# Performance work log

Hardware: AMD Instinct MI355X
Metric: run time of the kernel (lower is better)

Reference implementation:

```python
import jax, jax.numpy as jnp
import numpy as np

B, L, D = 2, 4096, 128      # batch, seq_len, d_model
ED = 2 * D                  # d_inner (expand=2) = 256
N = 16                      # d_state
K = 4                       # d_conv
R = (D + 15) // 16          # dt_rank = 8
H = 2 * D                   # mlp hidden = 256


def setup_inputs() -> dict:
    key = jax.random.key(0)
    ks = jax.random.split(key, 20)
    s = 0.05
    inp = {
        "x": jax.random.normal(ks[0], (B, L, D), dtype=jnp.float32),
        # outer block LayerNorm (norm1)
        "norm1_g": jnp.ones((D,), jnp.float32),
        "norm1_b": jnp.zeros((D,), jnp.float32),
        # MambaLayer inner LayerNorm
        "inner_g": jnp.ones((D,), jnp.float32),
        "inner_b": jnp.zeros((D,), jnp.float32),
        # Mamba params
        "in_w": jax.random.normal(ks[1], (2 * ED, D), jnp.float32) * s,      # in_proj (no bias)
        "conv_w": jax.random.normal(ks[2], (ED, 1, K), jnp.float32) * s,     # depthwise conv
        "conv_b": jax.random.normal(ks[3], (ED,), jnp.float32) * s,
        "xproj_w": jax.random.normal(ks[4], (R + 2 * N, ED), jnp.float32) * s,  # x_proj (no bias)
        "dt_w": jax.random.normal(ks[5], (ED, R), jnp.float32) * s,
        "dt_b": jax.random.normal(ks[6], (ED,), jnp.float32) * s,
        "A_log": jnp.tile(jnp.log(jnp.arange(1, N + 1, dtype=jnp.float32)), (ED, 1)),  # [ED,N]
        "Dp": jnp.ones((ED,), jnp.float32),
        "out_w": jax.random.normal(ks[7], (D, ED), jnp.float32) * s,         # out_proj (no bias)
        # MLP
        "fc1_w": jax.random.normal(ks[8], (H, D), jnp.float32) * s,
        "fc1_b": jnp.zeros((H,), jnp.float32),
        "fc2_w": jax.random.normal(ks[9], (D, H), jnp.float32) * s,
        "fc2_b": jnp.zeros((D,), jnp.float32),
    }
    return inp


def _ln(x, g, b, eps=1e-5):
    m = jnp.mean(x, axis=-1, keepdims=True)
    v = jnp.mean((x - m) ** 2, axis=-1, keepdims=True)
    return (x - m) * jax.lax.rsqrt(v + eps) * g + b


def _mamba(x, in_w, conv_w, conv_b, xproj_w, dt_w, dt_b, A_log, Dp, out_w):
    # x: [B, L, D]
    xz = jnp.einsum('bld,ed->ble', x, in_w)          # [B,L,2*ED]
    u, z = jnp.split(xz, 2, axis=-1)                 # each [B,L,ED]
    # causal depthwise conv1d over L
    u_c = jnp.transpose(u, (0, 2, 1))                # [B,ED,L]
    u_c = jax.lax.conv_general_dilated(
        u_c, conv_w, window_strides=(1,), padding=[(K - 1, 0)],
        dimension_numbers=('NCH', 'OIH', 'NCH'), feature_group_count=ED)
    u = jax.nn.silu(jnp.transpose(u_c, (0, 2, 1)) + conv_b)   # [B,L,ED]
    # input-dependent dt, B, C
    dbc = jnp.einsum('ble,re->blr', u, xproj_w)      # [B,L,R+2N]
    dt, Bm, Cm = jnp.split(dbc, [R, R + N], axis=-1)
    delta = jax.nn.softplus(jnp.einsum('blr,er->ble', dt, dt_w) + dt_b)  # [B,L,ED]
    A = -jnp.exp(A_log)                              # [ED,N]
    deltaA = jnp.exp(jnp.einsum('ble,en->blen', delta, A))               # [B,L,ED,N]
    deltaBu = jnp.einsum('ble,bln,ble->blen', delta, Bm, u)              # [B,L,ED,N]
    # selective scan over L
    def step(h, inp):
        dA, dBu, Ct = inp                            # [B,ED,N],[B,ED,N],[B,N]
        h = dA * h + dBu
        y = jnp.einsum('ben,bn->be', h, Ct)
        return h, y
    h0 = jnp.zeros((B, ED, N), u.dtype)
    xs = (jnp.transpose(deltaA, (1, 0, 2, 3)),
          jnp.transpose(deltaBu, (1, 0, 2, 3)),
          jnp.transpose(Cm, (1, 0, 2)))
    _, ys = jax.lax.scan(step, h0, xs)               # [L,B,ED]
    y = jnp.transpose(ys, (1, 0, 2)) + u * Dp        # [B,L,ED]
    y = y * jax.nn.silu(z)
    return jnp.einsum('ble,de->bld', y, out_w)       # [B,L,D]


def reference(x, norm1_g, norm1_b, inner_g, inner_b, in_w, conv_w, conv_b,
              xproj_w, dt_w, dt_b, A_log, Dp, out_w, fc1_w, fc1_b, fc2_w, fc2_b):
    # attn branch: mamba(inner_LN(norm1(x)))
    a = _mamba(_ln(_ln(x, norm1_g, norm1_b), inner_g, inner_b),
               in_w, conv_w, conv_b, xproj_w, dt_w, dt_b, A_log, Dp, out_w)
    x = x + a
    # mlp branch (note: original applies norm1 again to updated x)
    h = _ln(x, norm1_g, norm1_b)
    h = jax.nn.gelu(jnp.einsum('bld,hd->blh', h, fc1_w) + fc1_b, approximate=False)
    h = jnp.einsum('blh,dh->bld', h, fc2_w) + fc2_b
    return x + h
```

## Files before the change

kernel.cpp:

```cpp
#include <hip/hip_runtime.h>
#include <hip/hip_bf16.h>
#include <math.h>

#define BB 2
#define LL 4096
#define DD 128
#define ED 256
#define NN 16
#define KK 4
#define RR 8
#define HH 256
#define NT (BB*LL)
#define NC 128
#define LC 32
#define NCS 256
#define LCS 16

#define LOG2E 1.4426950408889634f

typedef __attribute__((ext_vector_type(8))) short short8;
typedef __attribute__((ext_vector_type(8))) unsigned short ushort8v;
typedef __attribute__((ext_vector_type(4))) float floatx4;

__device__ __forceinline__ unsigned short f2bf(float f) {
  unsigned int b = __builtin_bit_cast(unsigned int, f);
  b += 0x7FFFu + ((b >> 16) & 1u);
  return (unsigned short)(b >> 16);
}

__device__ __forceinline__ float exp2_fast(float x) {
#if __has_builtin(__builtin_amdgcn_exp2f)
  return __builtin_amdgcn_exp2f(x);
#else
  return exp2f(x);
#endif
}

__device__ __forceinline__ ushort8v pack8(const float4& v0, const float4& v1) {
  ushort8v p;
  p[0]=f2bf(v0.x); p[1]=f2bf(v0.y); p[2]=f2bf(v0.z); p[3]=f2bf(v0.w);
  p[4]=f2bf(v1.x); p[5]=f2bf(v1.y); p[6]=f2bf(v1.z); p[7]=f2bf(v1.w);
  return p;
}

#define S_IN  65536
#define S_XP  10240
#define S_OUT 32768
#define S_F1  32768
#define S_F2  32768
__global__ __launch_bounds__(256) void prep_k(
    const float* __restrict__ in_w, const float* __restrict__ xpw,
    const float* __restrict__ out_w, const float* __restrict__ fc1_w,
    const float* __restrict__ fc2_w, unsigned short* __restrict__ wb) {
  const int o = (blockIdx.x*256 + threadIdx.x) * 8;
  const float* src;
  int off;
  if (o < S_IN)                          { src = in_w;  off = o; }
  else if (o < S_IN+S_XP)                { src = xpw;   off = o - S_IN; }
  else if (o < S_IN+S_XP+S_OUT)          { src = out_w; off = o - S_IN - S_XP; }
  else if (o < S_IN+S_XP+S_OUT+S_F1)     { src = fc1_w; off = o - S_IN - S_XP - S_OUT; }
  else                                   { src = fc2_w; off = o - S_IN - S_XP - S_OUT - S_F1; }
  const float4 v0 = *(const float4*)(src + off);
  const float4 v1 = *(const float4*)(src + off + 4);
  *(ushort8v*)(wb + o) = pack8(v0, v1);
}

__global__ __launch_bounds__(512, 4) void scan1m_k(
    const float* __restrict__ x,
    const float* __restrict__ g1, const float* __restrict__ b1,
    const float* __restrict__ g2, const float* __restrict__ b2,
    const unsigned short* __restrict__ wb_in,
    const float* __restrict__ cw, const float* __restrict__ cb,
    const unsigned short* __restrict__ wb_xp,
    const float* __restrict__ dtw, const float* __restrict__ dtb,
    const float* __restrict__ A_log,
    float* __restrict__ uc, float* __restrict__ dbc,
    float* __restrict__ delta, float* __restrict__ gate,
    float* __restrict__ cA, float* __restrict__ cH) {
  __shared__ __align__(16) unsigned char SM[44624];
  auto Atile = reinterpret_cast<unsigned short(*)[136]>(SM);
  auto As    = reinterpret_cast<unsigned short(*)[264]>(SM);
  auto ubuf  = reinterpret_cast<float(*)[257]>(SM + 8704);
  auto sdbc  = reinterpret_cast<float(*)[40]>(SM + 8704);
  auto sus   = reinterpret_cast<float(*)[256]>(SM + 28240);

  const int c2 = blockIdx.x, b = blockIdx.y;
  const int tid = threadIdx.x;
  const int t0 = b*LL + c2*LCS;
  const int wave = tid >> 6, lane = tid & 63;
  const int quad = lane >> 4, l16 = lane & 15;

  {
    const int lr = tid >> 2, lk = (tid & 3) * 32;
    if (lr < 32) {
      if (lr < 19 && !(c2 == 0 && lr < 3)) {
        const float* Ap = x + (size_t)(t0 - 3 + lr)*DD + lk;
        float4 av[8];
        float s = 0.f, sq = 0.f;
        #pragma unroll
        for (int g = 0; g < 8; g++) {
          av[g] = *(const float4*)(Ap + g*4);
          s  += av[g].x + av[g].y + av[g].z + av[g].w;
          sq += av[g].x*av[g].x + av[g].y*av[g].y + av[g].z*av[g].z + av[g].w*av[g].w;
        }
        s += __shfl_xor(s, 1);  s += __shfl_xor(s, 2);
        sq += __shfl_xor(sq, 1); sq += __shfl_xor(sq, 2);
        const float m1 = s * (1.f/128.f);
        const float rs1 = rsqrtf(sq*(1.f/128.f) - m1*m1 + 1e-5f);
        float s2 = 0.f, sq2 = 0.f;
        #pragma unroll
        for (int g = 0; g < 8; g++) {
          const float4 gg = *(const float4*)(g1 + lk + g*4);
          const float4 bb = *(const float4*)(b1 + lk + g*4);
          av[g].x = (av[g].x - m1)*rs1*gg.x + bb.x;
          av[g].y = (av[g].y - m1)*rs1*gg.y + bb.y;
          av[g].z = (av[g].z - m1)*rs1*gg.z + bb.z;
          av[g].w = (av[g].w - m1)*rs1*gg.w + bb.w;
          s2  += av[g].x + av[g].y + av[g].z + av[g].w;
          sq2 += av[g].x*av[g].x + av[g].y*av[g].y + av[g].z*av[g].z + av[g].w*av[g].w;
        }
        s2 += __shfl_xor(s2, 1);  s2 += __shfl_xor(s2, 2);
        sq2 += __shfl_xor(sq2, 1); sq2 += __shfl_xor(sq2, 2);
        const float m2 = s2 * (1.f/128.f);
        const float rs2 = rsqrtf(sq2*(1.f/128.f) - m2*m2 + 1e-5f);
        #pragma unroll
        for (int g = 0; g < 4; g++) {
          const float4 ga = *(const float4*)(g2 + lk + g*8);
          const float4 gb = *(const float4*)(g2 + lk + g*8 + 4);
          const float4 ba = *(const float4*)(b2 + lk + g*8);
          const float4 bbv= *(const float4*)(b2 + lk + g*8 + 4);
          ushort8v pa;
          pa[0] = f2bf((av[2*g].x   - m2)*rs2*ga.x + ba.x);
          pa[1] = f2bf((av[2*g].y   - m2)*rs2*ga.y + ba.y);
          pa[2] = f2bf((av[2*g].z   - m2)*rs2*ga.z + ba.z);
          pa[3] = f2bf((av[2*g].w   - m2)*rs2*ga.w + ba.w);
          pa[4] = f2bf((av[2*g+1].x - m2)*rs2*gb.x + bbv.x);
          pa[5] = f2bf((av[2*g+1].y - m2)*rs2*gb.y + bbv.y);
          pa[6] = f2bf((av[2*g+1].z - m2)*rs2*gb.z + bbv.z);
          pa[7] = f2bf((av[2*g+1].w - m2)*rs2*gb.w + bbv.w);
          *(ushort8v*)&Atile[lr][lk + g*8] = pa;
        }
      } else {
        const ushort8v zz = {};
        #pragma unroll
        for (int g = 0; g < 4; g++) *(ushort8v*)&Atile[lr][lk + g*8] = zz;
      }
    }
  }
  __syncthreads();

  {
    const int mt = wave >> 2;
    short8 af[4];
    #pragma unroll
    for (int ks = 0; ks < 4; ks++)
      af[ks] = *(const short8*)&Atile[mt*16 + l16][ks*32 + quad*8];
    #pragma unroll
    for (int j = 0; j < 8; j++) {
      const int ncol = ((wave & 3)*8 + j) * 16;
      floatx4 acc = {};
      #pragma unroll
      for (int ks = 0; ks < 4; ks++) {
        short8 bv = *(const short8*)(wb_in + (size_t)(ncol + l16)*DD + ks*32 + quad*8);
        acc = __builtin_amdgcn_mfma_f32_16x16x32_bf16(af[ks], bv, acc, 0, 0, 0);
      }
      const int coll = ncol + l16;
      if (ncol < 256) {
        #pragma unroll
        for (int rr = 0; rr < 4; rr++) {
          const int m = mt*16 + quad*4 + rr;
          if (m < 19) ubuf[m][coll] = acc[rr];
        }
      } else {
        #pragma unroll
        for (int rr = 0; rr < 4; rr++) {
          const int m = mt*16 + quad*4 + rr;
          if (m >= 3 && m < 19) {
            const float v = acc[rr];
            gate[(size_t)(t0 + m - 3)*ED + coll - 256] = v / (1.f + __expf(-v));
          }
        }
      }
    }
  }
  __syncthreads();

  {
    const int ch = tid & 255, tg = tid >> 8;
    const int i0 = tg * 8;
    const float4 w = *(const float4*)(cw + ch*4);
    const float cbe = cb[ch];
    float v0 = ubuf[i0][ch], v1 = ubuf[i0+1][ch], v2 = ubuf[i0+2][ch];
    #pragma unroll
    for (int k = 0; k < 8; k++) {
      const float cur = ubuf[i0+3+k][ch];
      const float a = cbe + v0*w.x + v1*w.y + v2*w.z + cur*w.w;
      const float s = a / (1.f + __expf(-a));
      const int i = i0 + k;
      As[i][ch] = f2bf(s);
      sus[i][ch] = s;
      uc[(size_t)(t0+i)*ED + ch] = s;
      v0 = v1; v1 = v2; v2 = cur;
    }
  }
  __syncthreads();

  if (wave < 3) {
    const int jn = (wave == 2) ? 24 : wave*16;
    floatx4 acc = {};
    #pragma unroll
    for (int ks = 0; ks < 8; ks++) {
      const int ko = ks*32 + quad*8;
      short8 a  = *(const short8*)&As[l16][ko];
      short8 bv = *(const short8*)(wb_xp + (size_t)(jn + l16)*ED + ko);
      acc = __builtin_amdgcn_mfma_f32_16x16x32_bf16(a, bv, acc, 0, 0, 0);
    }
    const int n = jn + l16;
    if (wave < 2 || l16 >= 8) {
      #pragma unroll
      for (int rr = 0; rr < 4; rr++) {
        const int m = quad*4 + rr;
        sdbc[m][n] = acc[rr];
        dbc[(size_t)(t0 + m)*40 + n] = acc[rr];
      }
    }
  }
  __syncthreads();

  {
    const int e = tid >> 1, half = tid & 1;
    const int n0 = half * 8;
    const float4 dw0 = *(const float4*)(dtw + e*RR);
    const float4 dw1 = *(const float4*)(dtw + e*RR + 4);
    const float db = dtb[e];
    const float4 a0 = *(const float4*)(A_log + e*NN + n0);
    const float4 a1 = *(const float4*)(A_log + e*NN + n0 + 4);
    float Aen[8] = {-__expf(a0.x)*LOG2E, -__expf(a0.y)*LOG2E,
                    -__expf(a0.z)*LOG2E, -__expf(a0.w)*LOG2E,
                    -__expf(a1.x)*LOG2E, -__expf(a1.y)*LOG2E,
                    -__expf(a1.z)*LOG2E, -__expf(a1.w)*LOG2E};
    float h[8] = {};
    float sumd = 0.f;
    for (int t = 0; t < LCS; t++) {
      const float4 q0 = *(const float4*)&sdbc[t][0];
      const float4 q1 = *(const float4*)&sdbc[t][4];
      const float aa = db
          + q0.x*dw0.x + q0.y*dw0.y + q0.z*dw0.z + q0.w*dw0.w
          + q1.x*dw1.x + q1.y*dw1.y + q1.z*dw1.z + q1.w*dw1.w;
      const float dv = (aa > 20.f) ? aa : log1pf(__expf(aa));
      if (half == 0) delta[(size_t)(t0+t)*ED + e] = dv;
      const float du = dv * sus[t][e];
      const float4 B0 = *(const float4*)&sdbc[t][RR + n0];
      const float4 B1 = *(const float4*)&sdbc[t][RR + n0 + 4];
      const float Bv[8] = {B0.x,B0.y,B0.z,B0.w,B1.x,B1.y,B1.z,B1.w};
      sumd += dv;
      #pragma unroll
      for (int j = 0; j < 8; j++)
        h[j] = exp2_fast(dv * Aen[j])*h[j] + Bv[j]*du;
    }
    const size_t base = (((size_t)c2*BB + b)*ED + e)*NN + n0;
    *(float4*)(cA + base)     = make_float4(exp2_fast(sumd*Aen[0]), exp2_fast(sumd*Aen[1]),
                                            exp2_fast(sumd*Aen[2]), exp2_fast(sumd*Aen[3]));
    *(float4*)(cA + base + 4) = make_float4(exp2_fast(sumd*Aen[4]), exp2_fast(sumd*Aen[5]),
                                            exp2_fast(sumd*Aen[6]), exp2_fast(sumd*Aen[7]));
    *(float4*)(cH + base)     = make_float4(h[0], h[1], h[2], h[3]);
    *(float4*)(cH + base + 4) = make_float4(h[4], h[5], h[6], h[7]);
  }
}

__global__ __launch_bounds__(256) void scan2p8_k(float* __restrict__ cA,
    const float* __restrict__ cH) {
  const int gt = blockIdx.x*256 + threadIdx.x;
  const int scan = gt >> 3;
  const int seg  = gt & 7;
  const int lane = threadIdx.x & 63;
  const int lb   = lane & ~7;
  const int b = scan >> 12;
  const size_t base = (size_t)b*ED*NN + (scan & 4095);
  const int c0 = seg * 32;

  float ap = 1.f, hs = 0.f;
  for (int g = 0; g < 2; g++) {
    float av[16], hv[16];
    #pragma unroll
    for (int i = 0; i < 16; i++) {
      const size_t idx = (size_t)(c0 + g*16 + i)*(BB*ED*NN) + base;
      av[i] = cA[idx]; hv[i] = cH[idx];
    }
    #pragma unroll
    for (int i = 0; i < 16; i++) {
      hs = av[i]*hs + hv[i];
      ap *= av[i];
    }
  }
  float h = 0.f;
  #pragma unroll
  for (int k = 0; k < 7; k++) {
    const float ak = __shfl(ap, lb + k);
    const float hk = __shfl(hs, lb + k);
    if (seg > k) h = ak*h + hk;
  }
  for (int g = 0; g < 2; g++) {
    float av[16], hv[16];
    #pragma unroll
    for (int i = 0; i < 16; i++) {
      const size_t idx = (size_t)(c0 + g*16 + i)*(BB*ED*NN) + base;
      av[i] = cA[idx]; hv[i] = cH[idx];
    }
    #pragma unroll
    for (int i = 0; i < 16; i++) {
      const size_t idx = (size_t)(c0 + g*16 + i)*(BB*ED*NN) + base;
      cA[idx] = h;
      h = av[i]*h + hv[i];
    }
  }
}

__global__ __launch_bounds__(1024) void tail9_k(
    const float* __restrict__ gate, const float* __restrict__ delta,
    const float* __restrict__ uc, const float* __restrict__ dbc,
    const float* __restrict__ cP, const float* __restrict__ A_log,
    const float* __restrict__ Dpv, const float* __restrict__ x,
    const float* __restrict__ g1, const float* __restrict__ b1,
    const unsigned short* __restrict__ wb_out,
    const unsigned short* __restrict__ wb_f1,
    const unsigned short* __restrict__ wb_f2,
    const float* __restrict__ fc1_b, const float* __restrict__ fc2_b,
    float* __restrict__ out) {
  __shared__ __align__(16) unsigned short Au[32][264];
  __shared__ float xs[32][132];
  __shared__ float sbc[32][32];

  const int c = blockIdx.x, b = blockIdx.y;
  const int t0 = b*LL + c*LC;
  const int tid = threadIdx.x;
  const int wave = tid >> 6, lane = tid & 63;
  const int quad = lane >> 4, l16 = lane & 15;

  if (tid < 256) {
    const int row = tid >> 3, c4 = (tid & 7) * 4;
    *(float4*)&sbc[row][c4] = *(const float4*)(dbc + (size_t)(t0 + row)*40 + RR + c4);
  }
  __syncthreads();

  {
    const int e = tid >> 2, q = tid & 3;
    const int n0 = q * 4;
    float Aen[4], h[4];
    {
      const float4 a0 = *(const float4*)(A_log + e*NN + n0);
      Aen[0]=-__expf(a0.x)*LOG2E; Aen[1]=-__expf(a0.y)*LOG2E;
      Aen[2]=-__expf(a0.z)*LOG2E; Aen[3]=-__expf(a0.w)*LOG2E;
      const float4 h0 = *(const float4*)(cP + (((size_t)(2*c)*BB + b)*ED + e)*NN + n0);
      h[0]=h0.x; h[1]=h0.y; h[2]=h0.z; h[3]=h0.w;
    }
    const float Dpe = Dpv[e];
    float pd[8], pu[8], pg[8];
    #pragma unroll
    for (int i = 0; i < 8; i++) {
      pd[i] = delta[(size_t)(t0+i)*ED + e];
      pu[i] = uc[(size_t)(t0+i)*ED + e];
      pg[i] = gate[(size_t)(t0+i)*ED + e];
    }
    for (int g4 = 0; g4 < 4; g4++) {
      float cd[8], cu[8], cg[8];
      #pragma unroll
      for (int i = 0; i < 8; i++) { cd[i]=pd[i]; cu[i]=pu[i]; cg[i]=pg[i]; }
      if (g4 < 3) {
        const int tn = t0 + (g4+1)*8;
        #pragma unroll
        for (int i = 0; i < 8; i++) {
          pd[i] = delta[(size_t)(tn+i)*ED + e];
          pu[i] = uc[(size_t)(tn+i)*ED + e];
          pg[i] = gate[(size_t)(tn+i)*ED + e];
        }
      }
      #pragma unroll
      for (int i = 0; i < 8; i++) {
        const int t = g4*8 + i;
        const float dv = cd[i];
        const float uv = cu[i];
        const float du = dv * uv;
        const float4 B0 = *(const float4*)&sbc[t][n0];
        const float4 C0 = *(const float4*)&sbc[t][16 + n0];
        const float Bv[4] = {B0.x,B0.y,B0.z,B0.w};
        const float Cv[4] = {C0.x,C0.y,C0.z,C0.w};
        float part = 0.f;
        #pragma unroll
        for (int j = 0; j < 4; j++) {
          h[j] = exp2_fast(dv * Aen[j])*h[j] + Bv[j]*du;
          part += h[j]*Cv[j];
        }
        part += __shfl_xor(part, 1);
        part += __shfl_xor(part, 2);
        if (q == 0)
          Au[t][e] = f2bf((part + uv*Dpe) * cg[i]);
      }
    }
  }
  __syncthreads();

  {
    const int mi = (wave & 1) * 16;
    const int wn = (wave >> 1) * 16;
    floatx4 acc = {};
    #pragma unroll
    for (int ks = 0; ks < 8; ks++) {
      const int ko = ks*32 + quad*8;
      short8 a  = *(const short8*)&Au[mi + l16][ko];
      short8 bv = *(const short8*)(wb_out + (size_t)(wn + l16)*ED + ko);
      acc = __builtin_amdgcn_mfma_f32_16x16x32_bf16(a, bv, acc, 0, 0, 0);
    }
    const int n = wn + l16;
    #pragma unroll
    for (int r = 0; r < 4; r++) {
      const int m = mi + quad*4 + r;
      xs[m][n] = acc[r] + x[(size_t)(t0 + m)*DD + n];
    }
  }
  __syncthreads();

  if (tid < 512) {
    const int lr = tid >> 4, le = (tid & 15) * 8;
    float vv[8];
    float s = 0.f, sq = 0.f;
    #pragma unroll
    for (int i = 0; i < 8; i++) {
      vv[i] = xs[lr][le + i];
      s += vv[i]; sq += vv[i]*vv[i];
    }
    s += __shfl_xor(s, 1);  s += __shfl_xor(s, 2);
    s += __shfl_xor(s, 4);  s += __shfl_xor(s, 8);
    sq += __shfl_xor(sq, 1); sq += __shfl_xor(sq, 2);
    sq += __shfl_xor(sq, 4); sq += __shfl_xor(sq, 8);
    const float mean = s * (1.f/128.f);
    const float rs = rsqrtf(sq*(1.f/128.f) - mean*mean + 1e-5f);
    ushort8v p;
    #pragma unroll
    for (int i = 0; i < 8; i++)
      p[i] = f2bf((vv[i] - mean)*rs*g1[le + i] + b1[le + i]);
    *(ushort8v*)&Au[lr][le] = p;
  }
  __syncthreads();

  {
    const int mi = (wave & 1) * 16;
    const int wn = (wave >> 1) * 32;
    floatx4 acc[2] = {};
    #pragma unroll
    for (int ks = 0; ks < 4; ks++) {
      const int ko = ks*32 + quad*8;
      short8 a  = *(const short8*)&Au[mi + l16][ko];
      short8 b0 = *(const short8*)(wb_f1 + (size_t)(wn +      l16)*DD + ko);
      short8 b1v= *(const short8*)(wb_f1 + (size_t)(wn + 16 + l16)*DD + ko);
      acc[0] = __builtin_amdgcn_mfma_f32_16x16x32_bf16(a, b0, acc[0], 0, 0, 0);
      acc[1] = __builtin_amdgcn_mfma_f32_16x16x32_bf16(a, b1v, acc[1], 0, 0, 0);
    }
    __syncthreads();
    #pragma unroll
    for (int f = 0; f < 2; f++) {
      const int n = wn + f*16 + l16;
      const float bn = fc1_b[n];
      #pragma unroll
      for (int r = 0; r < 4; r++) {
        const int m = mi + quad*4 + r;
        float v = acc[f][r] + bn;
        v = 0.5f*v*(1.f + erff(v*0.70710678118f));
        Au[m][n] = f2bf(v);
      }
    }
  }
  __syncthreads();

  {
    const int mi = (wave & 1) * 16;
    const int wn = (wave >> 1) * 16;
    floatx4 acc = {};
    #pragma unroll
    for (int ks = 0; ks < 8; ks++) {
      const int ko = ks*32 + quad*8;
      short8 a  = *(const short8*)&Au[mi + l16][ko];
      short8 bv = *(const short8*)(wb_f2 + (size_t)(wn + l16)*HH + ko);
      acc = __builtin_amdgcn_mfma_f32_16x16x32_bf16(a, bv, acc, 0, 0, 0);
    }
    const int n = wn + l16;
    const float bn = fc2_b[n];
    #pragma unroll
    for (int r = 0; r < 4; r++) {
      const int m = mi + quad*4 + r;
      out[(size_t)(t0 + m)*DD + n] = acc[r] + bn + xs[m][n];
    }
  }
}

extern "C" void kernel_launch(void* const* d_in, const int* in_sizes, int n_in,
                              void* d_out, int out_size, void* d_ws, size_t ws_size,
                              hipStream_t stream) {
  const float* x      = (const float*)d_in[0];
  const float* n1g    = (const float*)d_in[1];
  const float* n1b    = (const float*)d_in[2];
  const float* ing    = (const float*)d_in[3];
  const float* inb    = (const float*)d_in[4];
  const float* in_w   = (const float*)d_in[5];
  const float* conv_w = (const float*)d_in[6];
  const float* conv_b = (const float*)d_in[7];
  const float* xproj_w= (const float*)d_in[8];
  const float* dt_w   = (const float*)d_in[9];
  const float* dt_b   = (const float*)d_in[10];
  const float* A_log  = (const float*)d_in[11];
  const float* Dpv    = (const float*)d_in[12];
  const float* out_w  = (const float*)d_in[13];
  const float* fc1_w  = (const float*)d_in[14];
  const float* fc1_b  = (const float*)d_in[15];
  const float* fc2_w  = (const float*)d_in[16];
  const float* fc2_b  = (const float*)d_in[17];
  float* out = (float*)d_out;

  float* ws    = (float*)d_ws;
  float* uc    = ws;
  float* dbc   = uc    + (size_t)NT*ED;
  float* delta = dbc   + (size_t)NT*40;
  float* gate  = delta + (size_t)NT*ED;
  float* cA    = gate  + (size_t)NT*ED;
  float* cH    = cA    + (size_t)NCS*BB*ED*NN;
  unsigned short* wb = (unsigned short*)(cH + (size_t)NCS*BB*ED*NN);
  unsigned short* wb_in  = wb;
  unsigned short* wb_xp  = wb_in  + S_IN;
  unsigned short* wb_out = wb_xp  + S_XP;
  unsigned short* wb_f1  = wb_out + S_OUT;
  unsigned short* wb_f2  = wb_f1  + S_F1;

  prep_k<<<(S_IN+S_XP+S_OUT+S_F1+S_F2)/(256*8), 256, 0, stream>>>(
      in_w, xproj_w, out_w, fc1_w, fc2_w, wb);
  scan1m_k<<<dim3(NCS, BB), 512, 0, stream>>>(x, n1g, n1b, ing, inb, wb_in,
                                              conv_w, conv_b, wb_xp, dt_w, dt_b,
                                              A_log, uc, dbc, delta, gate, cA, cH);
  scan2p8_k<<<(8*BB*ED*NN)/256, 256, 0, stream>>>(cA, cH);
  tail9_k<<<dim3(NC, BB), 1024, 0, stream>>>(gate, delta, uc, dbc, cA, A_log, Dpv,
                                             x, n1g, n1b, wb_out, wb_f1, wb_f2,
                                             fc1_b, fc2_b, out);
}
```

Baseline: 173.3 us.

## Rework scan1 LayerNorm mapping, share B fragments across M tiles, prefetch scan inputs

The LayerNorm prologue now uses 16 threads per row with 8 elements each, so all 512 threads take part instead of 128. In the in_proj MFMA stage each wave handles both 16-row M tiles, so one loaded B fragment from global memory feeds two MFMAs. This halves the weight reads per block and drops the row-32 padding work. The per-chunk scan loop prefetches the next timestep's LDS values into registers, and softplus now uses fast exp2 and log2 intrinsics instead of log1pf. The fast-math softplus can lose a little accuracy for very negative inputs.

```diff
diff --git a/kernel.cpp b/kernel.cpp
--- a/kernel.cpp
+++ b/kernel.cpp
@@ -17,6 +17,7 @@
 #define LCS 16
 
 #define LOG2E 1.4426950408889634f
+#define LN2F  0.6931471805599453f
 
 typedef __attribute__((ext_vector_type(8))) short short8;
 typedef __attribute__((ext_vector_type(8))) unsigned short ushort8v;
@@ -65,7 +66,7 @@
   *(ushort8v*)(wb + o) = pack8(v0, v1);
 }
 
-__global__ __launch_bounds__(512, 4) void scan1m_k(
+__global__ __launch_bounds__(512, 4) void scan1n_k(
     const float* __restrict__ x,
     const float* __restrict__ g1, const float* __restrict__ b1,
     const float* __restrict__ g2, const float* __restrict__ b2,
@@ -91,93 +92,107 @@
   const int quad = lane >> 4, l16 = lane & 15;
 
   {
-    const int lr = tid >> 2, lk = (tid & 3) * 32;
-    if (lr < 32) {
-      if (lr < 19 && !(c2 == 0 && lr < 3)) {
-        const float* Ap = x + (size_t)(t0 - 3 + lr)*DD + lk;
-        float4 av[8];
-        float s = 0.f, sq = 0.f;
+    const int lr = tid >> 4, le = (tid & 15) * 8;
+    if (lr < 19 && !(c2 == 0 && lr < 3)) {
+      const float* Ap = x + (size_t)(t0 - 3 + lr)*DD + le;
+      float4 a0 = *(const float4*)(Ap);
+      float4 a1 = *(const float4*)(Ap + 4);
+      float s  = a0.x + a0.y + a0.z + a0.w + a1.x + a1.y + a1.z + a1.w;
+      float sq = a0.x*a0.x + a0.y*a0.y + a0.z*a0.z + a0.w*a0.w
+               + a1.x*a1.x + a1.y*a1.y + a1.z*a1.z + a1.w*a1.w;
+      s += __shfl_xor(s, 1);  s += __shfl_xor(s, 2);
+      s += __shfl_xor(s, 4);  s += __shfl_xor(s, 8);
+      sq += __shfl_xor(sq, 1); sq += __shfl_xor(sq, 2);
+      sq += __shfl_xor(sq, 4); sq += __shfl_xor(sq, 8);
+      const float m1 = s * (1.f/128.f);
+      const float rs1 = rsqrtf(sq*(1.f/128.f) - m1*m1 + 1e-5f);
+      const float4 ga0 = *(const float4*)(g1 + le);
+      const float4 ga1 = *(const float4*)(g1 + le + 4);
+      const float4 bb0 = *(const float4*)(b1 + le);
+      const float4 bb1 = *(const float4*)(b1 + le + 4);
+      float4 v0, v1;
+      v0.x = (a0.x - m1)*rs1*ga0.x + bb0.x;
+      v0.y = (a0.y - m1)*rs1*ga0.y + bb0.y;
+      v0.z = (a0.z - m1)*rs1*ga0.z + bb0.z;
+      v0.w = (a0.w - m1)*rs1*ga0.w + bb0.w;
+      v1.x = (a1.x - m1)*rs1*ga1.x + bb1.x;
+      v1.y = (a1.y - m1)*rs1*ga1.y + bb1.y;
+      v1.z = (a1.z - m1)*rs1*ga1.z + bb1.z;
+      v1.w = (a1.w - m1)*rs1*ga1.w + bb1.w;
+      float s2  = v0.x + v0.y + v0.z + v0.w + v1.x + v1.y + v1.z + v1.w;
+      float sq2 = v0.x*v0.x + v0.y*v0.y + v0.z*v0.z + v0.w*v0.w
+                + v1.x*v1.x + v1.y*v1.y + v1.z*v1.z + v1.w*v1.w;
+      s2 += __shfl_xor(s2, 1);  s2 += __shfl_xor(s2, 2);
+      s2 += __shfl_xor(s2, 4);  s2 += __shfl_xor(s2, 8);
+      sq2 += __shfl_xor(sq2, 1); sq2 += __shfl_xor(sq2, 2);
+      sq2 += __shfl_xor(sq2, 4); sq2 += __shfl_xor(sq2, 8);
+      const float m2 = s2 * (1.f/128.f);
+      const float rs2 = rsqrtf(sq2*(1.f/128.f) - m2*m2 + 1e-5f);
+      const float4 gc0 = *(const float4*)(g2 + le);
+      const float4 gc1 = *(const float4*)(g2 + le + 4);
+      const float4 bc0 = *(const float4*)(b2 + le);
+      const float4 bc1 = *(const float4*)(b2 + le + 4);
+      ushort8v pa;
+      pa[0] = f2bf((v0.x - m2)*rs2*gc0.x + bc0.x);
+      pa[1] = f2bf((v0.y - m2)*rs2*gc0.y + bc0.y);
+      pa[2] = f2bf((v0.z - m2)*rs2*gc0.z + bc0.z);
+      pa[3] = f2bf((v0.w - m2)*rs2*gc0.w + bc0.w);
+      pa[4] = f2bf((v1.x - m2)*rs2*gc1.x + bc1.x);
+      pa[5] = f2bf((v1.y - m2)*rs2*gc1.y + bc1.y);
+      pa[6] = f2bf((v1.z - m2)*rs2*gc1.z + bc1.z);
+      pa[7] = f2bf((v1.w - m2)*rs2*gc1.w + bc1.w);
+      *(ushort8v*)&Atile[lr][le] = pa;
+    } else {
+      const ushort8v zz = {};
+      *(ushort8v*)&Atile[lr][le] = zz;
+    }
+  }
+  __syncthreads();
+
+  {
+    short8 af[2][4];
+    #pragma unroll
+    for (int mt = 0; mt < 2; mt++)
+      #pragma unroll
+      for (int ks = 0; ks < 4; ks++)
+        af[mt][ks] = *(const short8*)&Atile[mt*16 + l16][ks*32 + quad*8];
+    const int nb = wave * 64;
+    #pragma unroll
+    for (int j = 0; j < 4; j++) {
+      const int ncol = nb + j*16;
+      floatx4 acc0 = {}, acc1 = {};
+      #pragma unroll
+      for (int ks = 0; ks < 4; ks++) {
+        short8 bv = *(const short8*)(wb_in + (size_t)(ncol + l16)*DD + ks*32 + quad*8);
+        acc0 = __builtin_amdgcn_mfma_f32_16x16x32_bf16(af[0][ks], bv, acc0, 0, 0, 0);
+        acc1 = __builtin_amdgcn_mfma_f32_16x16x32_bf16(af[1][ks], bv, acc1, 0, 0, 0);
+      }
+      const int coll = ncol + l16;
+      if (nb < 256) {
         #pragma unroll
-        for (int g = 0; g < 8; g++) {
-          av[g] = *(const float4*)(Ap + g*4);
-          s  += av[g].x + av[g].y + av[g].z + av[g].w;
-          sq += av[g].x*av[g].x + av[g].y*av[g].y + av[g].z*av[g].z + av[g].w*av[g].w;
-        }
-        s += __shfl_xor(s, 1);  s += __shfl_xor(s, 2);
-        sq += __shfl_xor(sq, 1); sq += __shfl_xor(sq, 2);
-        const float m1 = s * (1.f/128.f);
-        const float rs1 = rsqrtf(sq*(1.f/128.f) - m1*m1 + 1e-5f);
-        float s2 = 0.f, sq2 = 0.f;
+        for (int rr = 0; rr < 4; rr++)
+          ubuf[quad*4 + rr][coll] = acc0[rr];
         #pragma unroll
-        for (int g = 0; g < 8; g++) {
-          const float4 gg = *(const float4*)(g1 + lk + g*4);
-          const float4 bb = *(const float4*)(b1 + lk + g*4);
-          av[g].x = (av[g].x - m1)*rs1*gg.x + bb.x;
-          av[g].y = (av[g].y - m1)*rs1*gg.y + bb.y;
-          av[g].z = (av[g].z - m1)*rs1*gg.z + bb.z;
-          av[g].w = (av[g].w - m1)*rs1*gg.w + bb.w;
-          s2  += av[g].x + av[g].y + av[g].z + av[g].w;
-          sq2 += av[g].x*av[g].x + av[g].y*av[g].y + av[g].z*av[g].z + av[g].w*av[g].w;
-        }
-        s2 += __shfl_xor(s2, 1);  s2 += __shfl_xor(s2, 2);
-        sq2 += __shfl_xor(sq2, 1); sq2 += __shfl_xor(sq2, 2);
-        const float m2 = s2 * (1.f/128.f);
-        const float rs2 = rsqrtf(sq2*(1.f/128.f) - m2*m2 + 1e-5f);
-        #pragma unroll
-        for (int g = 0; g < 4; g++) {
-          const float4 ga = *(const float4*)(g2 + lk + g*8);
-          const float4 gb = *(const float4*)(g2 + lk + g*8 + 4);
-          const float4 ba = *(const float4*)(b2 + lk + g*8);
-          const float4 bbv= *(const float4*)(b2 + lk + g*8 + 4);
-          ushort8v pa;
-          pa[0] = f2bf((av[2*g].x   - m2)*rs2*ga.x + ba.x);
-          pa[1] = f2bf((av[2*g].y   - m2)*rs2*ga.y + ba.y);
-          pa[2] = f2bf((av[2*g].z   - m2)*rs2*ga.z + ba.z);
-          pa[3] = f2bf((av[2*g].w   - m2)*rs2*ga.w + ba.w);
-          pa[4] = f2bf((av[2*g+1].x - m2)*rs2*gb.x + bbv.x);
-          pa[5] = f2bf((av[2*g+1].y - m2)*rs2*gb.y + bbv.y);
-          pa[6] = f2bf((av[2*g+1].z - m2)*rs2*gb.z + bbv.z);
-          pa[7] = f2bf((av[2*g+1].w - m2)*rs2*gb.w + bbv.w);
-          *(ushort8v*)&Atile[lr][lk + g*8] = pa;
+        for (int rr = 0; rr < 4; rr++) {
+          const int m = 16 + quad*4 + rr;
+          if (m < 19) ubuf[m][coll] = acc1[rr];
         }
       } else {
-        const ushort8v zz = {};
-        #pragma unroll
-        for (int g = 0; g < 4; g++) *(ushort8v*)&Atile[lr][lk + g*8] = zz;
-      }
-    }
-  }
-  __syncthreads();
-
-  {
-    const int mt = wave >> 2;
-    short8 af[4];
-    #pragma unroll
-    for (int ks = 0; ks < 4; ks++)
-      af[ks] = *(const short8*)&Atile[mt*16 + l16][ks*32 + quad*8];
-    #pragma unroll
-    for (int j = 0; j < 8; j++) {
-      const int ncol = ((wave & 3)*8 + j) * 16;
-      floatx4 acc = {};
-      #pragma unroll
-      for (int ks = 0; ks < 4; ks++) {
-        short8 bv = *(const short8*)(wb_in + (size_t)(ncol + l16)*DD + ks*32 + quad*8);
-        acc = __builtin_amdgcn_mfma_f32_16x16x32_bf16(af[ks], bv, acc, 0, 0, 0);
-      }
-      const int coll = ncol + l16;
-      if (ncol < 256) {
+        const int gcol = coll - 256;
         #pragma unroll
         for (int rr = 0; rr < 4; rr++) {
-          const int m = mt*16 + quad*4 + rr;
-          if (m < 19) ubuf[m][coll] = acc[rr];
+          const int m = quad*4 + rr;
+          if (m >= 3) {
+            const float v = acc0[rr];
+            gate[(size_t)(t0 + m - 3)*ED + gcol] = v / (1.f + __expf(-v));
+          }
         }
-      } else {
         #pragma unroll
         for (int rr = 0; rr < 4; rr++) {
-          const int m = mt*16 + quad*4 + rr;
-          if (m >= 3 && m < 19) {
-            const float v = acc[rr];
-            gate[(size_t)(t0 + m - 3)*ED + coll - 256] = v / (1.f + __expf(-v));
+          const int m = 16 + quad*4 + rr;
+          if (m < 19) {
+            const float v = acc1[rr];
+            gate[(size_t)(t0 + m - 3)*ED + gcol] = v / (1.f + __expf(-v));
           }
         }
       }
@@ -241,18 +256,33 @@
                     -__expf(a1.z)*LOG2E, -__expf(a1.w)*LOG2E};
     float h[8] = {};
     float sumd = 0.f;
+    float4 q0 = *(const float4*)&sdbc[0][0];
+    float4 q1 = *(const float4*)&sdbc[0][4];
+    float4 B0 = *(const float4*)&sdbc[0][RR + n0];
+    float4 B1 = *(const float4*)&sdbc[0][RR + n0 + 4];
+    float su = sus[0][e];
     for (int t = 0; t < LCS; t++) {
-      const float4 q0 = *(const float4*)&sdbc[t][0];
-      const float4 q1 = *(const float4*)&sdbc[t][4];
+      const float4 cq0 = q0, cq1 = q1, cB0 = B0, cB1 = B1;
+      const float csu = su;
+      if (t < LCS-1) {
+        q0 = *(const float4*)&sdbc[t+1][0];
+        q1 = *(const float4*)&sdbc[t+1][4];
+        B0 = *(const float4*)&sdbc[t+1][RR + n0];
+        B1 = *(const float4*)&sdbc[t+1][RR + n0 + 4];
+        su = sus[t+1][e];
+      }
       const float aa = db
-          + q0.x*dw0.x + q0.y*dw0.y + q0.z*dw0.z + q0.w*dw0.w
-          + q1.x*dw1.x + q1.y*dw1.y + q1.z*dw1.z + q1.w*dw1.w;
-      const float dv = (aa > 20.f) ? aa : log1pf(__expf(aa));
+          + cq0.x*dw0.x + cq0.y*dw0.y + cq0.z*dw0.z + cq0.w*dw0.w
+          + cq1.x*dw1.x + cq1.y*dw1.y + cq1.z*dw1.z + cq1.w*dw1.w;
+      float dv;
+      if (aa > 20.f) dv = aa;
+      else {
+        const float et = exp2_fast(aa * LOG2E);
+        dv = __log2f(1.f + et) * LN2F;
+      }
       if (half == 0) delta[(size_t)(t0+t)*ED + e] = dv;
-      const float du = dv * sus[t][e];
-      const float4 B0 = *(const float4*)&sdbc[t][RR + n0];
-      const float4 B1 = *(const float4*)&sdbc[t][RR + n0 + 4];
-      const float Bv[8] = {B0.x,B0.y,B0.z,B0.w,B1.x,B1.y,B1.z,B1.w};
+      const float du = dv * csu;
+      const float Bv[8] = {cB0.x,cB0.y,cB0.z,cB0.w, cB1.x,cB1.y,cB1.z,cB1.w};
       sumd += dv;
       #pragma unroll
       for (int j = 0; j < 8; j++)
@@ -532,7 +562,7 @@
 
   prep_k<<<(S_IN+S_XP+S_OUT+S_F1+S_F2)/(256*8), 256, 0, stream>>>(
       in_w, xproj_w, out_w, fc1_w, fc2_w, wb);
-  scan1m_k<<<dim3(NCS, BB), 512, 0, stream>>>(x, n1g, n1b, ing, inb, wb_in,
+  scan1n_k<<<dim3(NCS, BB), 512, 0, stream>>>(x, n1g, n1b, ing, inb, wb_in,
                                               conv_w, conv_b, wb_xp, dt_w, dt_b,
                                               A_log, uc, dbc, delta, gate, cA, cH);
   scan2p8_k<<<(8*BB*ED*NN)/256, 256, 0, stream>>>(cA, cH);
```

New measurement: 177.7 us. +2.5%, slower.
